# Kernel tuning notes

Measured on AMD Instinct MI355X. Metric: run time of the kernel, lower is better.

The kernel has to match this reference:

```python
import jax, jax.numpy as jnp
import numpy as np

B = 32768      # batch size
D = 256        # embedding dim
C = 2048       # number of classes (label range)
WEIGHT = 1.0
TEMPERATURE = 0.3
EPS = 1e-12


def setup_inputs() -> dict:
    key = jax.random.key(0)
    k1, k2 = jax.random.split(key)
    features = jax.random.normal(k1, (B, D), dtype=jnp.float32)
    labels = jax.random.randint(k2, (B,), 0, C, dtype=jnp.int32)
    return {"features": features, "labels": labels, "epoch": 5}


def reference(features, labels, epoch):
    # L2-normalize embeddings (F.normalize, p=2, dim=1)
    norms = jnp.sqrt(jnp.sum(features * features, axis=1, keepdims=True))
    f = features / jnp.maximum(norms, EPS)                      # [B, D]

    # per-class segment sums / counts (vectorized replacement of the python loop)
    ones = jnp.ones((f.shape[0],), dtype=f.dtype)
    counts = jax.ops.segment_sum(ones, labels, num_segments=C)  # [C]
    sums = jax.ops.segment_sum(f, labels, num_segments=C)       # [C, D]
    centroids = sums / jnp.maximum(counts, 1.0)[:, None]        # [C, D] (mean; empty classes masked later)

    # leave-one-out positive centroid: (sum_class - f_i) / (n_class - 1)
    cnt_i = counts[labels]                                       # [B]
    c_p = (sums[labels] - f) / jnp.maximum(cnt_i - 1.0, 1.0)[:, None]
    d_p = jnp.sqrt(jnp.sum((f - c_p) ** 2, axis=1) + EPS)        # [B]

    # distances to all class centroids: ||f||=1 after normalization
    cn2 = jnp.sum(centroids * centroids, axis=1)                 # [C]
    d2 = 1.0 + cn2[None, :] - 2.0 * (f @ centroids.T)           # [B, C]
    d = jnp.sqrt(jnp.maximum(d2, EPS))

    # mask own class and empty (absent-in-batch) classes, take min negative distance
    class_ids = jnp.arange(C, dtype=labels.dtype)
    neg_mask = (counts[None, :] > 0) & (labels[:, None] != class_ids[None, :])
    d_n = jnp.min(jnp.where(neg_mask, d, jnp.inf), axis=1)       # [B]

    # samples are skipped if their class is a singleton or no negative class exists
    valid = (cnt_i > 1.0) & jnp.isfinite(d_n)
    d_n_safe = jnp.where(jnp.isfinite(d_n), d_n, 0.0)

    # temperature schedule: min(temperature + 0.02*epoch, 1)
    temp = min(TEMPERATURE + 0.02 * epoch, 1.0)

    # ln(1 + exp((d_p - d_n)/t)) == softplus
    loss_per_sample = jax.nn.softplus((d_p - d_n_safe) / temp)
    cnt = jnp.sum(valid.astype(f.dtype))
    loss = jnp.where(cnt > 0,
                     jnp.sum(jnp.where(valid, loss_per_sample, 0.0)) / jnp.maximum(cnt, 1.0),
                     0.0)
    return WEIGHT * loss
```

## Files before the change

### kernel.cpp

```cpp
#include <hip/hip_runtime.h>
#include <hip/hip_bf16.h>
#include <math.h>

constexpr int Bn = 32768;
constexpr int Dn = 256;
constexpr int Cn = 2048;
constexpr int NSPLIT = 4;
constexpr int CLS_PER_BLK = Cn / NSPLIT;
constexpr int TCLS = 32;
constexpr int NIT = CLS_PER_BLK / TCLS;
#define EPSF 1e-12f
#define INFF __builtin_inff()

typedef __bf16 bf16x8 __attribute__((ext_vector_type(8)));
typedef __bf16 bf16x4 __attribute__((ext_vector_type(4)));
typedef float  f32x4  __attribute__((ext_vector_type(4)));

__device__ inline void async_copy16(const void* g, void* l) {
    __builtin_amdgcn_global_load_lds(
        (const __attribute__((address_space(1))) void*)g,
        (__attribute__((address_space(3))) void*)l, 16, 0, 0);
}

__global__ __launch_bounds__(256) void k_prep(const float* __restrict__ feat,
                                              __bf16* __restrict__ fneg) {
    const int wave = threadIdx.x >> 6, lane = threadIdx.x & 63;
    const int s = blockIdx.x * 4 + wave;
    const float4 v = ((const float4*)(feat + (size_t)s * Dn))[lane];
    float ss = v.x * v.x + v.y * v.y + v.z * v.z + v.w * v.w;
    #pragma unroll
    for (int off = 1; off < 64; off <<= 1) ss += __shfl_xor(ss, off, 64);
    const float inv = -2.0f / fmaxf(sqrtf(ss), EPSF);
    bf16x4 bf;
    bf[0] = (__bf16)(v.x * inv); bf[1] = (__bf16)(v.y * inv);
    bf[2] = (__bf16)(v.z * inv); bf[3] = (__bf16)(v.w * inv);
    *(bf16x4*)(fneg + (size_t)s * Dn + lane * 4) = bf;
}

__global__ __launch_bounds__(256) void k_sort(const int* __restrict__ labels,
                                              int* __restrict__ cnt_i,
                                              int* __restrict__ offs,
                                              int* __restrict__ order,
                                              float* __restrict__ accum,
                                              unsigned* __restrict__ donecnt) {
    __shared__ int sh_hist[Cn];
    __shared__ int part[256];
    const int t = threadIdx.x;
    for (int b = t; b < Cn; b += 256) sh_hist[b] = 0;
    if (t == 0) { accum[0] = 0.f; accum[1] = 0.f; *donecnt = 0u; }
    __syncthreads();
    const int4* lab4 = (const int4*)labels;
    for (int i = t; i < Bn / 4; i += 256) {
        const int4 l4 = lab4[i];
        atomicAdd(&sh_hist[l4.x], 1); atomicAdd(&sh_hist[l4.y], 1);
        atomicAdd(&sh_hist[l4.z], 1); atomicAdd(&sh_hist[l4.w], 1);
    }
    __syncthreads();
    int h[8], pre[8]; int sum = 0;
    #pragma unroll
    for (int j = 0; j < 8; ++j) { h[j] = sh_hist[t * 8 + j]; pre[j] = sum; sum += h[j]; }
    int v = sum;
    part[t] = v; __syncthreads();
    for (int off = 1; off < 256; off <<= 1) {
        int add = (t >= off) ? part[t - off] : 0;
        __syncthreads();
        v += add; part[t] = v;
        __syncthreads();
    }
    const int base = v - sum;
    #pragma unroll
    for (int j = 0; j < 8; ++j) {
        const int b = t * 8 + j, o = base + pre[j];
        cnt_i[b] = h[j]; offs[b] = o; sh_hist[b] = o;
    }
    __syncthreads();
    for (int i = t; i < Bn; i += 256) {
        const int l = labels[i];
        const int pos = atomicAdd(&sh_hist[l], 1);
        order[pos] = i;
    }
}

__global__ __launch_bounds__(256) void k_centseg(const __bf16* __restrict__ fneg,
                                                 const int* __restrict__ order,
                                                 const int* __restrict__ offs,
                                                 const int* __restrict__ cnt_i,
                                                 __bf16* __restrict__ centK,
                                                 float* __restrict__ cn2x) {
    const int wave = threadIdx.x >> 6, lane = threadIdx.x & 63;
    const int c = blockIdx.x * 4 + wave;
    const int n = cnt_i[c], start = offs[c];
    int myidx = 0;
    if (lane < n) myidx = order[start + lane];
    float sx = 0.f, sy = 0.f, sz = 0.f, sw = 0.f;
    const int nf = (n < 64) ? n : 64;
    for (int j = 0; j < nf; ++j) {
        const int idx = __shfl(myidx, j, 64);
        const bf16x4 v = *(const bf16x4*)(fneg + (size_t)idx * Dn + lane * 4);
        sx += -0.5f * (float)v[0]; sy += -0.5f * (float)v[1];
        sz += -0.5f * (float)v[2]; sw += -0.5f * (float)v[3];
    }
    for (int j = 64; j < n; ++j) {
        const int idx = order[start + j];
        const bf16x4 v = *(const bf16x4*)(fneg + (size_t)idx * Dn + lane * 4);
        sx += -0.5f * (float)v[0]; sy += -0.5f * (float)v[1];
        sz += -0.5f * (float)v[2]; sw += -0.5f * (float)v[3];
    }
    const float invn = 1.0f / fmaxf((float)n, 1.0f);
    const float cx = sx * invn, cy = sy * invn, cz = sz * invn, cw = sw * invn;
    bf16x4 cb; cb[0] = (__bf16)cx; cb[1] = (__bf16)cy; cb[2] = (__bf16)cz; cb[3] = (__bf16)cw;
    *(bf16x4*)(centK + ((size_t)(lane >> 1) * Cn + c) * 8 + (lane & 1) * 4) = cb;
    float ss = cx * cx + cy * cy + cz * cz + cw * cw;
    #pragma unroll
    for (int off = 1; off < 64; off <<= 1) ss += __shfl_xor(ss, off, 64);
    if (lane == 0) cn2x[c] = (n > 0) ? ss : INFF;
}

__global__ __launch_bounds__(256, 2) void k_main(const __bf16* __restrict__ fneg,
                                                 const int* __restrict__ labels,
                                                 const __bf16* __restrict__ centK,
                                                 const float* __restrict__ cn2x,
                                                 float* __restrict__ minval,
                                                 float* __restrict__ dotown) {
    __shared__ __align__(16) __bf16 sB[2][TCLS * Dn];
    __shared__ float s_cn2[CLS_PER_BLK];
    const int lane = threadIdx.x & 63, wave = threadIdx.x >> 6;
    const int m16 = lane & 15, quad = lane >> 4;
    const int sbase = blockIdx.x * 256 + wave * 64;
    const int c_begin = blockIdx.y * CLS_PER_BLK;

    bf16x8 a[4][8];
    #pragma unroll
    for (int p = 0; p < 4; ++p) {
        const __bf16* fr = fneg + (size_t)(sbase + p * 16 + m16) * Dn + quad * 8;
        #pragma unroll
        for (int t = 0; t < 8; ++t) a[p][t] = *(const bf16x8*)(fr + t * 32);
    }
    int lab[4][4];
    #pragma unroll
    for (int p = 0; p < 4; ++p)
        #pragma unroll
        for (int r = 0; r < 4; ++r)
            lab[p][r] = labels[sbase + p * 16 + quad * 4 + r];

    float rm[4][4], dacc[4][4];
    #pragma unroll
    for (int p = 0; p < 4; ++p)
        #pragma unroll
        for (int r = 0; r < 4; ++r) { rm[p][r] = INFF; dacc[p][r] = 0.0f; }

    auto stage = [&](int buf, int it) {
        const int c0 = c_begin + it * TCLS;
        #pragma unroll
        for (int j = 0; j < 4; ++j) {
            const int chunk = wave * 256 + j * 64 + lane;
            const int h  = chunk >> 9;
            const int kc = (chunk >> 4) & 31;
            const int n  = chunk & 15;
            const __bf16* g = centK + ((size_t)kc * Cn + (c0 + h * 16 + n)) * 8;
            __bf16* l = &sB[buf][(size_t)(wave * 256 + j * 64) * 8];
            async_copy16(g, l);
        }
    };

    stage(0, 0);
    for (int c = threadIdx.x; c < CLS_PER_BLK; c += 256) s_cn2[c] = cn2x[c_begin + c];
    __syncthreads();
    for (int it = 0; it < NIT; ++it) {
        const int cur = it & 1;
        if (it + 1 < NIT) stage(cur ^ 1, it + 1);
        #pragma unroll
        for (int hh = 0; hh < 2; ++hh) {
            const int ctile = it * TCLS + hh * 16;
            const float cn2v = s_cn2[ctile + m16];
            const __bf16* ls = &sB[cur][hh * 4096];
            f32x4 acc[4] = {{0.f,0.f,0.f,0.f},{0.f,0.f,0.f,0.f},
                            {0.f,0.f,0.f,0.f},{0.f,0.f,0.f,0.f}};
            #pragma unroll
            for (int t = 0; t < 8; ++t) {
                const bf16x8 b = *(const bf16x8*)(ls + t * 512 + lane * 8);
                #pragma unroll
                for (int p = 0; p < 4; ++p)
                    acc[p] = __builtin_amdgcn_mfma_f32_16x16x32_bf16(a[p][t], b, acc[p], 0, 0, 0);
            }
            const int crow = c_begin + ctile + m16;
            #pragma unroll
            for (int p = 0; p < 4; ++p)
                #pragma unroll
                for (int r = 0; r < 4; ++r) {
                    const bool own = (crow == lab[p][r]);
                    const float sel = own ? INFF : cn2v;
                    rm[p][r] = fminf(rm[p][r], sel + acc[p][r]);
                    dacc[p][r] += own ? acc[p][r] : 0.0f;
                }
        }
        __syncthreads();
    }
    #pragma unroll
    for (int off = 1; off < 16; off <<= 1)
        #pragma unroll
        for (int p = 0; p < 4; ++p)
            #pragma unroll
            for (int r = 0; r < 4; ++r) {
                rm[p][r] = fminf(rm[p][r], __shfl_xor(rm[p][r], off, 64));
                dacc[p][r] += __shfl_xor(dacc[p][r], off, 64);
            }
    if (m16 == 0) {
        float* mv = minval + (size_t)blockIdx.y * Bn;
        float* dv = dotown + (size_t)blockIdx.y * Bn;
        #pragma unroll
        for (int p = 0; p < 4; ++p)
            #pragma unroll
            for (int r = 0; r < 4; ++r) {
                mv[sbase + p * 16 + quad * 4 + r] = rm[p][r];
                dv[sbase + p * 16 + quad * 4 + r] = dacc[p][r];
            }
    }
}

__global__ __launch_bounds__(256) void k_final(const int* __restrict__ labels,
                                               const int* __restrict__ cnt_i,
                                               const float* __restrict__ cn2x,
                                               const float* __restrict__ minval,
                                               const float* __restrict__ dotown,
                                               const int* __restrict__ epoch,
                                               float* __restrict__ accum,
                                               unsigned* __restrict__ donecnt,
                                               float* __restrict__ out) {
    const int i = blockIdx.x * 256 + threadIdx.x;
    const int lane = threadIdx.x & 63;
    const float temp = fminf(0.3f + 0.02f * (float)(*epoch), 1.0f);
    float m = minval[i];
    float draw = dotown[i];
    #pragma unroll
    for (int k = 1; k < NSPLIT; ++k) {
        m = fminf(m, minval[(size_t)k * Bn + i]);
        draw += dotown[(size_t)k * Bn + i];
    }
    const int l = labels[i];
    const int n = cnt_i[l];
    const float nf = (float)n;
    const float cn2 = cn2x[l];
    const float fds = nf * (-0.5f * draw);
    const float fm1 = fmaxf(nf - 1.0f, 1.0f);
    const float fdcp = (fds - 1.0f) / fm1;
    const float cp2 = (nf * nf * cn2 - 2.0f * fds + 1.0f) / (fm1 * fm1);
    const float dp2 = 1.0f - 2.0f * fdcp + cp2;
    const float d_p = sqrtf(fmaxf(dp2, 0.0f) + EPSF);
    const bool finite = (m < 1e37f);
    const float d_n = finite ? sqrtf(fmaxf(1.0f + m, EPSF)) : 0.0f;
    const bool valid = (n > 1) && finite;
    const float x = (d_p - d_n) / temp;
    const float sp = fmaxf(x, 0.0f) + log1pf(expf(-fabsf(x)));
    float ws = valid ? sp : 0.0f, wc = valid ? 1.0f : 0.0f;
    #pragma unroll
    for (int off = 1; off < 64; off <<= 1) {
        ws += __shfl_xor(ws, off, 64);
        wc += __shfl_xor(wc, off, 64);
    }
    if (lane == 0) {
        atomicAdd(&accum[0], ws);
        atomicAdd(&accum[1], wc);
        __threadfence();
    }
    __syncthreads();
    if (threadIdx.x == 0) {
        const unsigned old = atomicAdd(donecnt, 1u);
        if (old == (unsigned)(gridDim.x - 1)) {
            __threadfence();
            const float s = __hip_atomic_load(&accum[0], __ATOMIC_RELAXED,
                                              __HIP_MEMORY_SCOPE_AGENT);
            const float c = __hip_atomic_load(&accum[1], __ATOMIC_RELAXED,
                                              __HIP_MEMORY_SCOPE_AGENT);
            out[0] = (c > 0.0f) ? (s / fmaxf(c, 1.0f)) : 0.0f;
        }
    }
}

extern "C" void kernel_launch(void* const* d_in, const int* in_sizes, int n_in,
                              void* d_out, int out_size, void* d_ws, size_t ws_size,
                              hipStream_t stream) {
    const float* feat  = (const float*)d_in[0];
    const int* labels  = (const int*)d_in[1];
    const int* epoch   = (const int*)d_in[2];
    float* out = (float*)d_out;
    char* ws = (char*)d_ws;

    size_t off = 0;
    __bf16* fneg     = (__bf16*)(ws + off); off += (size_t)Bn * Dn * 2;
    __bf16* centK    = (__bf16*)(ws + off); off += (size_t)Cn * Dn * 2;
    float*  cn2x     = (float*)(ws + off);  off += (size_t)Cn * 4;
    int*    cnt_i    = (int*)(ws + off);    off += (size_t)Cn * 4;
    int*    offs     = (int*)(ws + off);    off += (size_t)Cn * 4;
    int*    order    = (int*)(ws + off);    off += (size_t)Bn * 4;
    float*  minval   = (float*)(ws + off);  off += (size_t)NSPLIT * Bn * 4;
    float*  dotown   = (float*)(ws + off);  off += (size_t)NSPLIT * Bn * 4;
    float*  accum    = (float*)(ws + off);  off += 2 * 4;
    unsigned* donecnt = (unsigned*)(ws + off); off += 4;

    k_prep<<<Bn / 4, 256, 0, stream>>>(feat, fneg);
    k_sort<<<1, 256, 0, stream>>>(labels, cnt_i, offs, order, accum, donecnt);
    k_centseg<<<Cn / 4, 256, 0, stream>>>(fneg, order, offs, cnt_i, centK, cn2x);
    dim3 g5(Bn / 256, NSPLIT);
    k_main<<<g5, 256, 0, stream>>>(fneg, labels, centK, cn2x, minval, dotown);
    k_final<<<Bn / 256, 256, 0, stream>>>(labels, cnt_i, cn2x, minval, dotown,
                                          epoch, accum, donecnt, out);
}
```

Baseline: 198.2 us.

## Replace single-block counting sort with per-class ballot scan of labels

Removes the single-block k_sort kernel that built a histogram, prefix sum and order array. Each class wave in k_centseg now scans the full label array with ballots to find its members, counts them and accumulates their features directly. This drops a serial one-block launch and its dependency, but every wave now reads all 32K labels (128KB), about 2048×128KB of mostly L2-cached traffic in total.

```diff
diff --git a/kernel.cpp b/kernel.cpp
--- a/kernel.cpp
+++ b/kernel.cpp
@@ -37,75 +37,42 @@
     *(bf16x4*)(fneg + (size_t)s * Dn + lane * 4) = bf;
 }
 
-__global__ __launch_bounds__(256) void k_sort(const int* __restrict__ labels,
-                                              int* __restrict__ cnt_i,
-                                              int* __restrict__ offs,
-                                              int* __restrict__ order,
-                                              float* __restrict__ accum,
-                                              unsigned* __restrict__ donecnt) {
-    __shared__ int sh_hist[Cn];
-    __shared__ int part[256];
-    const int t = threadIdx.x;
-    for (int b = t; b < Cn; b += 256) sh_hist[b] = 0;
-    if (t == 0) { accum[0] = 0.f; accum[1] = 0.f; *donecnt = 0u; }
-    __syncthreads();
-    const int4* lab4 = (const int4*)labels;
-    for (int i = t; i < Bn / 4; i += 256) {
-        const int4 l4 = lab4[i];
-        atomicAdd(&sh_hist[l4.x], 1); atomicAdd(&sh_hist[l4.y], 1);
-        atomicAdd(&sh_hist[l4.z], 1); atomicAdd(&sh_hist[l4.w], 1);
-    }
-    __syncthreads();
-    int h[8], pre[8]; int sum = 0;
-    #pragma unroll
-    for (int j = 0; j < 8; ++j) { h[j] = sh_hist[t * 8 + j]; pre[j] = sum; sum += h[j]; }
-    int v = sum;
-    part[t] = v; __syncthreads();
-    for (int off = 1; off < 256; off <<= 1) {
-        int add = (t >= off) ? part[t - off] : 0;
-        __syncthreads();
-        v += add; part[t] = v;
-        __syncthreads();
-    }
-    const int base = v - sum;
-    #pragma unroll
-    for (int j = 0; j < 8; ++j) {
-        const int b = t * 8 + j, o = base + pre[j];
-        cnt_i[b] = h[j]; offs[b] = o; sh_hist[b] = o;
-    }
-    __syncthreads();
-    for (int i = t; i < Bn; i += 256) {
-        const int l = labels[i];
-        const int pos = atomicAdd(&sh_hist[l], 1);
-        order[pos] = i;
-    }
-}
-
 __global__ __launch_bounds__(256) void k_centseg(const __bf16* __restrict__ fneg,
-                                                 const int* __restrict__ order,
-                                                 const int* __restrict__ offs,
-                                                 const int* __restrict__ cnt_i,
+                                                 const int* __restrict__ labels,
+                                                 int* __restrict__ cnt_i,
                                                  __bf16* __restrict__ centK,
-                                                 float* __restrict__ cn2x) {
+                                                 float* __restrict__ cn2x,
+                                                 float* __restrict__ accum,
+                                                 unsigned* __restrict__ donecnt) {
     const int wave = threadIdx.x >> 6, lane = threadIdx.x & 63;
     const int c = blockIdx.x * 4 + wave;
-    const int n = cnt_i[c], start = offs[c];
-    int myidx = 0;
-    if (lane < n) myidx = order[start + lane];
+    if (blockIdx.x == 0 && threadIdx.x == 0) {
+        accum[0] = 0.f; accum[1] = 0.f; *donecnt = 0u;
+    }
     float sx = 0.f, sy = 0.f, sz = 0.f, sw = 0.f;
-    const int nf = (n < 64) ? n : 64;
-    for (int j = 0; j < nf; ++j) {
-        const int idx = __shfl(myidx, j, 64);
-        const bf16x4 v = *(const bf16x4*)(fneg + (size_t)idx * Dn + lane * 4);
-        sx += -0.5f * (float)v[0]; sy += -0.5f * (float)v[1];
-        sz += -0.5f * (float)v[2]; sw += -0.5f * (float)v[3];
-    }
-    for (int j = 64; j < n; ++j) {
-        const int idx = order[start + j];
-        const bf16x4 v = *(const bf16x4*)(fneg + (size_t)idx * Dn + lane * 4);
-        sx += -0.5f * (float)v[0]; sy += -0.5f * (float)v[1];
-        sz += -0.5f * (float)v[2]; sw += -0.5f * (float)v[3];
-    }
+    int cnt = 0;
+    const int4* lab4 = (const int4*)labels;
+    for (int ch = 0; ch < Bn / 256; ++ch) {
+        const int4 l4 = lab4[ch * 64 + lane];
+        unsigned long long b0 = __ballot(l4.x == c);
+        unsigned long long b1 = __ballot(l4.y == c);
+        unsigned long long b2 = __ballot(l4.z == c);
+        unsigned long long b3 = __ballot(l4.w == c);
+        cnt += __popcll(b0) + __popcll(b1) + __popcll(b2) + __popcll(b3);
+        const int base = ch * 256;
+        #pragma unroll
+        for (int w = 0; w < 4; ++w) {
+            unsigned long long b = (w == 0) ? b0 : (w == 1) ? b1 : (w == 2) ? b2 : b3;
+            while (b) {
+                const int s = __ffsll(b) - 1; b &= b - 1;
+                const int idx = base + 4 * s + w;
+                const bf16x4 v = *(const bf16x4*)(fneg + (size_t)idx * Dn + lane * 4);
+                sx += -0.5f * (float)v[0]; sy += -0.5f * (float)v[1];
+                sz += -0.5f * (float)v[2]; sw += -0.5f * (float)v[3];
+            }
+        }
+    }
+    const int n = cnt;
     const float invn = 1.0f / fmaxf((float)n, 1.0f);
     const float cx = sx * invn, cy = sy * invn, cz = sz * invn, cw = sw * invn;
     bf16x4 cb; cb[0] = (__bf16)cx; cb[1] = (__bf16)cy; cb[2] = (__bf16)cz; cb[3] = (__bf16)cw;
@@ -113,7 +80,10 @@
     float ss = cx * cx + cy * cy + cz * cz + cw * cw;
     #pragma unroll
     for (int off = 1; off < 64; off <<= 1) ss += __shfl_xor(ss, off, 64);
-    if (lane == 0) cn2x[c] = (n > 0) ? ss : INFF;
+    if (lane == 0) {
+        cn2x[c] = (n > 0) ? ss : INFF;
+        cnt_i[c] = n;
+    }
 }
 
 __global__ __launch_bounds__(256, 2) void k_main(const __bf16* __restrict__ fneg,
@@ -291,16 +261,14 @@
     __bf16* centK    = (__bf16*)(ws + off); off += (size_t)Cn * Dn * 2;
     float*  cn2x     = (float*)(ws + off);  off += (size_t)Cn * 4;
     int*    cnt_i    = (int*)(ws + off);    off += (size_t)Cn * 4;
-    int*    offs     = (int*)(ws + off);    off += (size_t)Cn * 4;
-    int*    order    = (int*)(ws + off);    off += (size_t)Bn * 4;
     float*  minval   = (float*)(ws + off);  off += (size_t)NSPLIT * Bn * 4;
     float*  dotown   = (float*)(ws + off);  off += (size_t)NSPLIT * Bn * 4;
     float*  accum    = (float*)(ws + off);  off += 2 * 4;
     unsigned* donecnt = (unsigned*)(ws + off); off += 4;
 
     k_prep<<<Bn / 4, 256, 0, stream>>>(feat, fneg);
-    k_sort<<<1, 256, 0, stream>>>(labels, cnt_i, offs, order, accum, donecnt);
-    k_centseg<<<Cn / 4, 256, 0, stream>>>(fneg, order, offs, cnt_i, centK, cn2x);
+    k_centseg<<<Cn / 4, 256, 0, stream>>>(fneg, labels, cnt_i, centK, cn2x,
+                                          accum, donecnt);
     dim3 g5(Bn / 256, NSPLIT);
     k_main<<<g5, 256, 0, stream>>>(fneg, labels, centK, cn2x, minval, dotown);
     k_final<<<Bn / 256, 256, 0, stream>>>(labels, cnt_i, cn2x, minval, dotown,
```

New measurement: 184.1 us. -7.1%, faster.
